# Optimization experiments

Measured on AMD Instinct MI355X. Metric: run time of the kernel, lower is better.

The kernel has to match this reference:

```python
import jax, jax.numpy as jnp
import numpy as np

PAD, UNK, END = 0, 1, 2  # per tgt_map init kwarg


def setup_inputs() -> dict:
    key = jax.random.key(0)
    k1, k2, k3, k4 = jax.random.split(key, 4)
    B, L, V = 16, 512, 32000
    # logits are consumed as probabilities (-log(p) directly); keep them in (1e-3, 1)
    logits = jax.random.uniform(k1, (B, L, V), dtype=jnp.float32, minval=1e-3, maxval=1.0)
    forwarded_trgs = jax.random.randint(k2, (B, L), 0, 50, dtype=jnp.int64)
    targets = jax.random.randint(k3, (B, L), 0, V, dtype=jnp.int64)
    sequence_lengths = jax.random.randint(k4, (B,), 0, L - 3, dtype=jnp.int64)
    inserted = jnp.zeros((B,), dtype=jnp.int64)
    return {
        "logits": logits,
        "forwarded_trgs": forwarded_trgs,
        "targets": targets,
        "sequence_lengths": sequence_lengths,
        "inserted": inserted,
    }


def reference(logits, forwarded_trgs, targets, sequence_lengths, inserted):
    # Positions strictly before the first <PAD> (the Python loop breaks at PAD)
    valid = jnp.cumsum((forwarded_trgs == PAD).astype(jnp.int32), axis=1) == 0  # [B,L]
    unk = valid & (forwarded_trgs == UNK)                                       # [B,L]

    # tag_to_insert = targets[i-1]; at i==0 torch negative indexing wraps to targets[-1]
    prev_tgt = jnp.roll(targets, 1, axis=1)                                     # [B,L]
    p = jnp.take_along_axis(logits, prev_tgt[:, :, None], axis=2)[:, :, 0]      # [B,L]
    nll = -jnp.log(p)

    cnt = jnp.sum(unk.astype(jnp.float32), axis=1)                              # [B]
    sent_mean = jnp.sum(jnp.where(unk, nll, 0.0), axis=1) / jnp.maximum(cnt, 1.0)

    # Fallback when no UNK found before PAD: -log(logits[seq_len+2, <END>])
    fb_p = jnp.take_along_axis(logits[:, :, END], (sequence_lengths + 2)[:, None], axis=1)[:, 0]
    sent_loss = jnp.where(cnt > 0, sent_mean, -jnp.log(fb_p))                   # [B]

    # Rows with inserted >= seq_len are skipped; batch loss = mean over active rows
    active = (inserted < sequence_lengths).astype(jnp.float32)                  # [B]
    loss = jnp.sum(sent_loss * active) / jnp.maximum(jnp.sum(active), 1.0)
    return loss
```

## Files before the change

### kernel.cpp

```cpp
#include <hip/hip_runtime.h>

#define PAD_TOK 0
#define UNK_TOK 1
#define END_TOK 2

__global__ __launch_bounds__(1024) void ti_loss_fused_kernel(
    const float* __restrict__ logits,
    const int*   __restrict__ fwd,
    const int*   __restrict__ tgt,
    const int*   __restrict__ seqlen,
    const int*   __restrict__ inserted,
    float*       __restrict__ out,
    int B, int L, int V)
{
    const int t    = threadIdx.x;
    const int wid  = t >> 6;
    const int lane = t & 63;
    const int nw   = blockDim.x >> 6;

    __shared__ float s_val[32];
    __shared__ float s_act[32];

    for (int b = wid; b < B; b += nw) {
        const int*   frow = fwd + (size_t)b * L;
        const int*   trow = tgt + (size_t)b * L;
        const float* lrow = logits + (size_t)b * L * V;

        int4 v[4];
        int niter = 0;
        for (int base = 4 * lane; base < L; base += 256) {
            v[niter++] = *(const int4*)(frow + base);
        }

        int lfp = L;
        for (int k = 0; k < niter; ++k) {
            const int base = 4 * lane + k * 256;
            if (v[k].x == PAD_TOK) lfp = min(lfp, base + 0);
            if (v[k].y == PAD_TOK) lfp = min(lfp, base + 1);
            if (v[k].z == PAD_TOK) lfp = min(lfp, base + 2);
            if (v[k].w == PAD_TOK) lfp = min(lfp, base + 3);
        }
        #pragma unroll
        for (int off = 32; off > 0; off >>= 1)
            lfp = min(lfp, __shfl_xor(lfp, off));
        const int fp = lfp;

        float sum = 0.f, cnt = 0.f;
        for (int k = 0; k < niter; ++k) {
            const int base = 4 * lane + k * 256;
            const int vals[4] = { v[k].x, v[k].y, v[k].z, v[k].w };
            #pragma unroll
            for (int j = 0; j < 4; ++j) {
                const int i = base + j;
                if (i < fp && vals[j] == UNK_TOK) {
                    const int pt = (i == 0) ? trow[L - 1] : trow[i - 1];
                    sum -= logf(lrow[(size_t)i * V + pt]);
                    cnt += 1.f;
                }
            }
        }
        #pragma unroll
        for (int off = 32; off > 0; off >>= 1) {
            sum += __shfl_xor(sum, off);
            cnt += __shfl_xor(cnt, off);
        }

        if (lane == 0) {
            float sent;
            if (cnt > 0.f) {
                sent = sum / cnt;
            } else {
                const int sl = seqlen[b];
                sent = -logf(lrow[(size_t)(sl + 2) * V + END_TOK]);
            }
            const float act = (inserted[b] < seqlen[b]) ? 1.f : 0.f;
            s_val[b] = sent * act;
            s_act[b] = act;
        }
    }
    __syncthreads();

    if (t == 0) {
        float s = 0.f, a = 0.f;
        for (int b = 0; b < B; ++b) { s += s_val[b]; a += s_act[b]; }
        out[0] = s / fmaxf(a, 1.f);
    }
}

extern "C" void kernel_launch(void* const* d_in, const int* in_sizes, int n_in,
                              void* d_out, int out_size, void* d_ws, size_t ws_size,
                              hipStream_t stream) {
    const float* logits   = (const float*)d_in[0];
    const int*   fwd      = (const int*)d_in[1];
    const int*   tgt      = (const int*)d_in[2];
    const int*   seqlen   = (const int*)d_in[3];
    const int*   inserted = (const int*)d_in[4];
    float* out = (float*)d_out;

    const int B = in_sizes[3];
    const int L = in_sizes[1] / B;
    const int V = in_sizes[0] / (B * L);

    const int waves   = (B < 16) ? B : 16;
    const int threads = 64 * waves;

    ti_loss_fused_kernel<<<1, threads, 0, stream>>>(
        logits, fwd, tgt, seqlen, inserted, out, B, L, V);
}
```

Measured before the change: 10.26 us.

## Prefetch targets and gathered logits up front with compile-time L specialization

Specializes the kernel on the sequence length so loops fully unroll. It loads target rows as int4 vectors and derives each previous target through wave shuffles, where the old code issued a dependent scalar load. All UNK-position logit gathers and the fallback END logit are issued speculatively before the PAD scan, so the random global loads overlap instead of serializing after the reduction. The cost is extra gathers for UNK tokens past the first PAD and higher register use; a generic fallback kernel handles other lengths.

```diff
diff --git a/kernel.cpp b/kernel.cpp
--- a/kernel.cpp
+++ b/kernel.cpp
@@ -4,41 +4,79 @@
 #define UNK_TOK 1
 #define END_TOK 2
 
-__global__ __launch_bounds__(1024) void ti_loss_fused_kernel(
+template<int NITER>
+__global__ __launch_bounds__(1024) void ti_loss_fused_tpl(
     const float* __restrict__ logits,
     const int*   __restrict__ fwd,
     const int*   __restrict__ tgt,
     const int*   __restrict__ seqlen,
     const int*   __restrict__ inserted,
     float*       __restrict__ out,
-    int B, int L, int V)
+    int B, int V)
 {
+    constexpr int L = NITER * 256;
     const int t    = threadIdx.x;
     const int wid  = t >> 6;
     const int lane = t & 63;
     const int nw   = blockDim.x >> 6;
 
-    __shared__ float s_val[32];
-    __shared__ float s_act[32];
+    __shared__ float s_val[64];
+    __shared__ float s_act[64];
 
     for (int b = wid; b < B; b += nw) {
         const int*   frow = fwd + (size_t)b * L;
         const int*   trow = tgt + (size_t)b * L;
         const float* lrow = logits + (size_t)b * L * V;
 
-        int4 v[4];
-        int niter = 0;
-        for (int base = 4 * lane; base < L; base += 256) {
-            v[niter++] = *(const int4*)(frow + base);
+        const int sl  = seqlen[b];
+        const int ins = inserted[b];
+        const float fbp = lrow[(size_t)(sl + 2) * V + END_TOK];
+
+        int4 fv[NITER], tv[NITER];
+        #pragma unroll
+        for (int k = 0; k < NITER; ++k) {
+            fv[k] = *(const int4*)(frow + 4 * lane + k * 256);
+            tv[k] = *(const int4*)(trow + 4 * lane + k * 256);
+        }
+
+        int pt[NITER][4];
+        #pragma unroll
+        for (int k = 0; k < NITER; ++k) {
+            const int kprev  = (k == 0) ? (NITER - 1) : (k - 1);
+            const int up_w   = __shfl_up(tv[k].w, 1);
+            const int wrap_w = __shfl(tv[kprev].w, 63);
+            pt[k][0] = (lane == 0) ? wrap_w : up_w;
+            pt[k][1] = tv[k].x;
+            pt[k][2] = tv[k].y;
+            pt[k][3] = tv[k].z;
+        }
+
+        int fvals[NITER][4];
+        #pragma unroll
+        for (int k = 0; k < NITER; ++k) {
+            fvals[k][0] = fv[k].x; fvals[k][1] = fv[k].y;
+            fvals[k][2] = fv[k].z; fvals[k][3] = fv[k].w;
+        }
+
+        float pv[NITER][4];
+        #pragma unroll
+        for (int k = 0; k < NITER; ++k) {
+            #pragma unroll
+            for (int j = 0; j < 4; ++j) {
+                const int i = 4 * lane + k * 256 + j;
+                pv[k][j] = (fvals[k][j] == UNK_TOK)
+                         ? lrow[(size_t)i * V + pt[k][j]] : 1.0f;
+            }
         }
 
         int lfp = L;
-        for (int k = 0; k < niter; ++k) {
-            const int base = 4 * lane + k * 256;
-            if (v[k].x == PAD_TOK) lfp = min(lfp, base + 0);
-            if (v[k].y == PAD_TOK) lfp = min(lfp, base + 1);
-            if (v[k].z == PAD_TOK) lfp = min(lfp, base + 2);
-            if (v[k].w == PAD_TOK) lfp = min(lfp, base + 3);
+        #pragma unroll
+        for (int k = 0; k < NITER; ++k) {
+            #pragma unroll
+            for (int j = 0; j < 4; ++j) {
+                const int i = 4 * lane + k * 256 + j;
+                if (fvals[k][j] == PAD_TOK) lfp = min(lfp, i);
+            }
         }
         #pragma unroll
         for (int off = 32; off > 0; off >>= 1)
@@ -46,15 +84,13 @@
         const int fp = lfp;
 
         float sum = 0.f, cnt = 0.f;
-        for (int k = 0; k < niter; ++k) {
-            const int base = 4 * lane + k * 256;
-            const int vals[4] = { v[k].x, v[k].y, v[k].z, v[k].w };
+        #pragma unroll
+        for (int k = 0; k < NITER; ++k) {
             #pragma unroll
             for (int j = 0; j < 4; ++j) {
-                const int i = base + j;
-                if (i < fp && vals[j] == UNK_TOK) {
-                    const int pt = (i == 0) ? trow[L - 1] : trow[i - 1];
-                    sum -= logf(lrow[(size_t)i * V + pt]);
+                const int i = 4 * lane + k * 256 + j;
+                if (i < fp && fvals[k][j] == UNK_TOK) {
+                    sum -= logf(pv[k][j]);
                     cnt += 1.f;
                 }
             }
@@ -66,24 +102,73 @@
         }
 
         if (lane == 0) {
-            float sent;
-            if (cnt > 0.f) {
-                sent = sum / cnt;
-            } else {
-                const int sl = seqlen[b];
-                sent = -logf(lrow[(size_t)(sl + 2) * V + END_TOK]);
-            }
-            const float act = (inserted[b] < seqlen[b]) ? 1.f : 0.f;
+            const float sent = (cnt > 0.f) ? (sum / cnt) : -logf(fbp);
+            const float act  = (ins < sl) ? 1.f : 0.f;
             s_val[b] = sent * act;
             s_act[b] = act;
         }
     }
     __syncthreads();
 
-    if (t == 0) {
-        float s = 0.f, a = 0.f;
-        for (int b = 0; b < B; ++b) { s += s_val[b]; a += s_act[b]; }
-        out[0] = s / fmaxf(a, 1.f);
+    if (t < 64) {
+        float v_ = (lane < B) ? s_val[lane] : 0.f;
+        float a_ = (lane < B) ? s_act[lane] : 0.f;
+        #pragma unroll
+        for (int off = 32; off > 0; off >>= 1) {
+            v_ += __shfl_xor(v_, off);
+            a_ += __shfl_xor(a_, off);
+        }
+        if (lane == 0) out[0] = v_ / fmaxf(a_, 1.f);
+    }
+}
+
+__global__ __launch_bounds__(1024) void ti_loss_fused_gen(
+    const float* __restrict__ logits, const int* __restrict__ fwd,
+    const int* __restrict__ tgt, const int* __restrict__ seqlen,
+    const int* __restrict__ inserted, float* __restrict__ out,
+    int B, int L, int V)
+{
+    const int t = threadIdx.x, wid = t >> 6, lane = t & 63, nw = blockDim.x >> 6;
+    __shared__ float s_val[64];
+    __shared__ float s_act[64];
+    for (int b = wid; b < B; b += nw) {
+        const int* frow = fwd + (size_t)b * L;
+        const int* trow = tgt + (size_t)b * L;
+        const float* lrow = logits + (size_t)b * L * V;
+        int lfp = L;
+        for (int i = lane; i < L; i += 64)
+            if (frow[i] == PAD_TOK) lfp = min(lfp, i);
+        #pragma unroll
+        for (int off = 32; off > 0; off >>= 1) lfp = min(lfp, __shfl_xor(lfp, off));
+        const int fp = lfp;
+        float sum = 0.f, cnt = 0.f;
+        for (int i = lane; i < L; i += 64) {
+            if (i < fp && frow[i] == UNK_TOK) {
+                const int ptg = (i == 0) ? trow[L - 1] : trow[i - 1];
+                sum -= logf(lrow[(size_t)i * V + ptg]);
+                cnt += 1.f;
+            }
+        }
+        #pragma unroll
+        for (int off = 32; off > 0; off >>= 1) {
+            sum += __shfl_xor(sum, off); cnt += __shfl_xor(cnt, off);
+        }
+        if (lane == 0) {
+            float sent = (cnt > 0.f) ? (sum / cnt)
+                                     : -logf(lrow[(size_t)(seqlen[b] + 2) * V + END_TOK]);
+            const float act = (inserted[b] < seqlen[b]) ? 1.f : 0.f;
+            s_val[b] = sent * act; s_act[b] = act;
+        }
+    }
+    __syncthreads();
+    if (t < 64) {
+        float v_ = (lane < B) ? s_val[lane] : 0.f;
+        float a_ = (lane < B) ? s_act[lane] : 0.f;
+        #pragma unroll
+        for (int off = 32; off > 0; off >>= 1) {
+            v_ += __shfl_xor(v_, off); a_ += __shfl_xor(a_, off);
+        }
+        if (lane == 0) out[0] = v_ / fmaxf(a_, 1.f);
     }
 }
 
@@ -104,6 +189,17 @@
     const int waves   = (B < 16) ? B : 16;
     const int threads = 64 * waves;
 
-    ti_loss_fused_kernel<<<1, threads, 0, stream>>>(
-        logits, fwd, tgt, seqlen, inserted, out, B, L, V);
+    if (L == 512) {
+        ti_loss_fused_tpl<2><<<1, threads, 0, stream>>>(
+            logits, fwd, tgt, seqlen, inserted, out, B, V);
+    } else if (L == 256) {
+        ti_loss_fused_tpl<1><<<1, threads, 0, stream>>>(
+            logits, fwd, tgt, seqlen, inserted, out, B, V);
+    } else if (L == 1024) {
+        ti_loss_fused_tpl<4><<<1, threads, 0, stream>>>(
+            logits, fwd, tgt, seqlen, inserted, out, B, V);
+    } else {
+        ti_loss_fused_gen<<<1, threads, 0, stream>>>(
+            logits, fwd, tgt, seqlen, inserted, out, B, L, V);
+    }
 }
```

Result: faster. 9.739 us (-5.1%).
